# Kernel tuning notes

Hardware: AMD Instinct MI355X
Metric: run time of the kernel (lower is better)

The kernel has to match this reference:

```python
import jax, jax.numpy as jnp
import numpy as np

N_SEQ = 250000
L = 40
C_IN = 20
K = 4
D = 32
N_BAGS = 100
SEQ_PER_BAG = N_SEQ // N_BAGS


def _param(key, shape):
    # matches torch init: normal(0, sqrt(1/prod(shape)))
    return jax.random.normal(key, shape, dtype=jnp.float32) * np.sqrt(1.0 / np.prod(shape))


def setup_inputs() -> dict:
    key = jax.random.key(0)
    ks = jax.random.split(key, 16)
    inp = {
        "x": jax.random.normal(ks[0], (N_SEQ, L, C_IN), dtype=jnp.float32),
        # equal-size bags: 100 bags of 2500 sequences (sum == N_SEQ)
        "n_per_bag": jnp.full((N_BAGS,), SEQ_PER_BAG, dtype=jnp.int32),
        # CNN: two conv1d layers, kernel shape (K, in, out) for 'NWC'/'WIO'
        "conv1_w": _param(ks[1], (K, C_IN, D)), "conv1_b": jnp.zeros((D,), jnp.float32),
        "conv2_w": _param(ks[2], (K, D, D)),    "conv2_b": jnp.zeros((D,), jnp.float32),
        # attention MLP: 32->32->32->1
        "att_w1": _param(ks[3], (D, D)), "att_b1": jnp.zeros((D,), jnp.float32),
        "att_w2": _param(ks[4], (D, D)), "att_b2": jnp.zeros((D,), jnp.float32),
        "att_w3": _param(ks[5], (D, 1)), "att_b3": jnp.zeros((1,), jnp.float32),
        # output net A: 32->32->21, output net B: 32->32->40
        "outA_w1": _param(ks[6], (D, D)),  "outA_b1": jnp.zeros((D,), jnp.float32),
        "outA_w2": _param(ks[7], (D, 21)), "outA_b2": jnp.zeros((21,), jnp.float32),
        "outB_w1": _param(ks[8], (D, D)),  "outB_b1": jnp.zeros((D,), jnp.float32),
        "outB_w2": _param(ks[9], (D, 40)), "outB_b2": jnp.zeros((40,), jnp.float32),
    }
    return inp


def _conv1d_nwc(x, w, b):
    # x: (N, L, Cin), w: (K, Cin, Cout) -> (N, L-K+1, Cout), VALID padding
    return jax.lax.conv_general_dilated(
        x, w, window_strides=(1,), padding="VALID",
        dimension_numbers=("NWC", "WIO", "NWC")) + b


def _forward(x, n_per_bag, conv1_w, conv1_b, conv2_w, conv2_b,
             att_w1, att_b1, att_w2, att_b2, att_w3, att_b3,
             outA_w1, outA_b1, outA_w2, outA_b2,
             outB_w1, outB_b1, outB_w2, outB_b2):
    selu = jax.nn.selu
    # --- sequence embedding CNN (dropout = identity in eval) ---
    h = selu(_conv1d_nwc(x, conv1_w, conv1_b))          # (N, L-3, D)
    h = selu(_conv1d_nwc(h, conv2_w, conv2_b))          # (N, L-6, D)
    seq_embed = h.max(axis=1)                           # (N, D)
    # --- attention scores ---
    a = selu(seq_embed @ att_w1 + att_b1)
    a = selu(a @ att_w2 + att_b2)
    scores = (a @ att_w3 + att_b3)[:, 0]                # (N,)
    # --- per-bag segment softmax + weighted-sum pooling ---
    seg = jnp.repeat(jnp.arange(N_BAGS, dtype=jnp.int32), np.asarray(n_per_bag),
                     total_repeat_length=seq_embed.shape[0])
    seg_max = jax.ops.segment_max(scores, seg, num_segments=N_BAGS)
    e = jnp.exp(scores - seg_max[seg])
    denom = jax.ops.segment_sum(e, seg, num_segments=N_BAGS)
    w = e / denom[seg]                                  # (N,)
    pooled = jax.ops.segment_sum(seq_embed * w[:, None], seg,
                                 num_segments=N_BAGS)   # (N_BAGS, D)
    # --- output networks (n_layers=2: one hidden SELU layer + final, then sigmoid) ---
    pa = jax.nn.sigmoid(selu(pooled @ outA_w1 + outA_b1) @ outA_w2 + outA_b2)
    pb = jax.nn.sigmoid(selu(pooled @ outB_w1 + outB_b1) @ outB_w2 + outB_b2)
    return pa, pb


def reference(x, n_per_bag, conv1_w, conv1_b, conv2_w, conv2_b,
              att_w1, att_b1, att_w2, att_b2, att_w3, att_b3,
              outA_w1, outA_b1, outA_w2, outA_b2,
              outB_w1, outB_b1, outB_w2, outB_b2):
    return _forward(x, n_per_bag, conv1_w, conv1_b, conv2_w, conv2_b,
                    att_w1, att_b1, att_w2, att_b2, att_w3, att_b3,
                    outA_w1, outA_b1, outA_w2, outA_b2,
                    outB_w1, outB_b1, outB_w2, outB_b2)
```

## Files before the change

kernel.cpp:

```cpp
#include <hip/hip_runtime.h>

#define N_SEQ 250000
#define LSEQ  40
#define CIN   20
#define KW    4
#define DCH   32
#define L1    37
#define L2    34
#define N_BAGS 100
#define SPB   2500
#define S_BLK 8
#define R1    (S_BLK * L1)
#define R2    (S_BLK * L2)
#define T1C   10
#define T2C   9
#define H1S   36
#define H2S   33

typedef _Float16 f16;
typedef _Float16 f16x8 __attribute__((ext_vector_type(8)));
typedef _Float16 f16x4 __attribute__((ext_vector_type(4)));
typedef float    f32x16 __attribute__((ext_vector_type(16)));

__device__ __forceinline__ float selu_f(float x) {
  float e = 1.6732632423543772f * (__expf(x) - 1.0f);
  return 1.0507009873554805f * ((x > 0.0f) ? x : e);
}

__global__ __launch_bounds__(256) void prep_kernel(
    const float* __restrict__ w1, const float* __restrict__ w2,
    const float* __restrict__ aw1, const float* __restrict__ aw2,
    f16* __restrict__ w1T, f16* __restrict__ w2T,
    float* __restrict__ aw1T, float* __restrict__ aw2T)
{
  const int tid = threadIdx.x;
  for (int i = tid; i < 32 * 80; i += 256) {
    const int n = i / 80, k = i - n * 80;
    w1T[i] = (f16)w1[k * 32 + n];
  }
  for (int i = tid; i < 32 * 128; i += 256) {
    const int n = i >> 7, k = i & 127;
    w2T[i] = (f16)w2[k * 32 + n];
  }
  for (int i = tid; i < 1024; i += 256) {
    const int d = i >> 5, c = i & 31;
    aw1T[i] = aw1[c * 32 + d];
    aw2T[i] = aw2[c * 32 + d];
  }
}

__global__ __launch_bounds__(256, 4) void seq_kernel(
    const float* __restrict__ x,
    const f16*  __restrict__ w1T, const float* __restrict__ b1,
    const f16*  __restrict__ w2T, const float* __restrict__ b2,
    const float* __restrict__ aw1T, const float* __restrict__ ab1,
    const float* __restrict__ aw2T, const float* __restrict__ ab2,
    const float* __restrict__ aw3, const float* __restrict__ ab3,
    f16* __restrict__ se_out, float* __restrict__ sc_out)
{
  __shared__ __align__(16) f16 reg1[R2 * H2S];
  __shared__ __align__(16) f16 reg2[R1 * H1S];

  f16* xs = reg1;
  f16* h2 = reg1;
  f16* h1 = reg2;
  float* sebuf = (float*)reg2;
  float* abuf  = sebuf + 256;

  const int tid  = threadIdx.x;
  const int lane = tid & 63;
  const int wave = tid >> 6;
  const int m    = lane & 31;
  const int half = lane >> 5;
  const int seq0 = blockIdx.x * S_BLK;

  f16x8 bf1[5], bf2[8];
  {
    const f16x8* w1t8 = (const f16x8*)w1T;
    const f16x8* w2t8 = (const f16x8*)w2T;
    #pragma unroll
    for (int kc = 0; kc < 5; kc++) bf1[kc] = w1t8[m * 10 + kc * 2 + half];
    #pragma unroll
    for (int kc = 0; kc < 8; kc++) bf2[kc] = w2t8[m * 16 + kc * 2 + half];
  }
  const float b1v = b1[m], b2v = b2[m];

  {
    const float4* xg = (const float4*)(x + (size_t)blockIdx.x * (S_BLK * LSEQ * CIN));
    for (int i = tid; i < S_BLK * LSEQ * CIN / 4; i += 256) {
      const float4 v = xg[i];
      f16x4 h; h[0] = (f16)v.x; h[1] = (f16)v.y; h[2] = (f16)v.z; h[3] = (f16)v.w;
      *(f16x4*)&xs[i * 4] = h;
    }
  }
  __syncthreads();

  for (int tile = wave; tile < T1C; tile += 4) {
    const unsigned r  = tile * 32 + m;
    const unsigned rc = (r < R1) ? r : (R1 - 1);
    const unsigned s  = rc / L1, l = rc - s * L1;
    const f16* arow = &xs[(s * LSEQ + l) * CIN];
    f32x16 acc;
    #pragma unroll
    for (int i = 0; i < 16; i++) acc[i] = b1v;
    #pragma unroll
    for (int kc = 0; kc < 5; kc++) {
      const int e = kc * 16 + half * 8;
      const f16x4 p0 = *(const f16x4*)(arow + e);
      const f16x4 p1 = *(const f16x4*)(arow + e + 4);
      const f16x8 a = __builtin_shufflevector(p0, p1, 0, 1, 2, 3, 4, 5, 6, 7);
      acc = __builtin_amdgcn_mfma_f32_32x32x16_f16(a, bf1[kc], acc, 0, 0, 0);
    }
    #pragma unroll
    for (int reg = 0; reg < 16; reg++) {
      const int rr = tile * 32 + (reg & 3) + 8 * (reg >> 2) + 4 * half;
      if (rr < R1) h1[rr * H1S + m] = (f16)selu_f(acc[reg]);
    }
  }
  __syncthreads();

  for (int tile = wave; tile < T2C; tile += 4) {
    const unsigned r  = tile * 32 + m;
    const unsigned rc = (r < R2) ? r : (R2 - 1);
    const unsigned s  = rc / L2, l = rc - s * L2;
    const f16* abase = &h1[(s * L1 + l) * H1S];
    f32x16 acc;
    #pragma unroll
    for (int i = 0; i < 16; i++) acc[i] = b2v;
    #pragma unroll
    for (int kc = 0; kc < 8; kc++) {
      const int e = (kc >> 1) * H1S + (kc & 1) * 16 + half * 8;
      const f16x4 p0 = *(const f16x4*)(abase + e);
      const f16x4 p1 = *(const f16x4*)(abase + e + 4);
      const f16x8 a = __builtin_shufflevector(p0, p1, 0, 1, 2, 3, 4, 5, 6, 7);
      acc = __builtin_amdgcn_mfma_f32_32x32x16_f16(a, bf2[kc], acc, 0, 0, 0);
    }
    #pragma unroll
    for (int reg = 0; reg < 16; reg++) {
      const int rr = tile * 32 + (reg & 3) + 8 * (reg >> 2) + 4 * half;
      if (rr < R2) h2[rr * H2S + m] = (f16)acc[reg];
    }
  }
  __syncthreads();

  {
    const int s = tid >> 5, d = tid & 31;
    float mx = -3.4e38f;
    for (int l = 0; l < L2; l++) mx = fmaxf(mx, (float)h2[(s * L2 + l) * H2S + d]);
    const float sv = selu_f(mx);
    sebuf[tid] = sv;
    se_out[(size_t)seq0 * DCH + tid] = (f16)sv;
  }
  __syncthreads();

  {
    const int s = tid >> 5, d = tid & 31;
    const float4* wt = (const float4*)aw1T;
    float a = ab1[d];
    #pragma unroll
    for (int c4 = 0; c4 < 8; c4++) {
      const float4 w = wt[d * 8 + c4];
      const float* sb = &sebuf[s * DCH + c4 * 4];
      a = fmaf(sb[0], w.x, a); a = fmaf(sb[1], w.y, a);
      a = fmaf(sb[2], w.z, a); a = fmaf(sb[3], w.w, a);
    }
    abuf[tid] = selu_f(a);
  }
  __syncthreads();

  {
    const int s = tid >> 5, d = tid & 31;
    const float4* wt = (const float4*)aw2T;
    float a = ab2[d];
    #pragma unroll
    for (int c4 = 0; c4 < 8; c4++) {
      const float4 w = wt[d * 8 + c4];
      const float* sb = &abuf[s * DCH + c4 * 4];
      a = fmaf(sb[0], w.x, a); a = fmaf(sb[1], w.y, a);
      a = fmaf(sb[2], w.z, a); a = fmaf(sb[3], w.w, a);
    }
    a = selu_f(a);
    float p = a * aw3[d];
    #pragma unroll
    for (int off = 16; off > 0; off >>= 1) p += __shfl_xor(p, off, 32);
    if (d == 0) sc_out[seq0 + s] = p + ab3[0];
  }
}

__global__ __launch_bounds__(256) void bag_kernel(
    const f16* __restrict__ se, const float* __restrict__ sc,
    const float* __restrict__ aw1, const float* __restrict__ ab1,
    const float* __restrict__ aw2, const float* __restrict__ ab2,
    const float* __restrict__ bw1, const float* __restrict__ bb1,
    const float* __restrict__ bw2, const float* __restrict__ bb2,
    float* __restrict__ out)
{
  const int bag = blockIdx.x, tid = threadIdx.x;
  const size_t base = (size_t)bag * SPB;

  __shared__ float pr[4][33];
  __shared__ float red[33];
  __shared__ float pool[DCH], hA[DCH], hB[DCH];

  float m = -3.4e38f;
  for (int i = tid; i < SPB; i += 256) m = fmaxf(m, sc[base + i]);
  #pragma unroll
  for (int off = 32; off > 0; off >>= 1) m = fmaxf(m, __shfl_xor(m, off, 64));
  if ((tid & 63) == 0) pr[tid >> 6][0] = m;
  __syncthreads();
  const float bagmax = fmaxf(fmaxf(pr[0][0], pr[1][0]), fmaxf(pr[2][0], pr[3][0]));
  __syncthreads();

  float acc[33];
  #pragma unroll
  for (int d = 0; d < 33; d++) acc[d] = 0.0f;
  for (int i = tid; i < SPB; i += 256) {
    const float e = __expf(sc[base + i] - bagmax);
    acc[32] += e;
    const f16* sr = &se[(base + i) * DCH];
    #pragma unroll
    for (int q = 0; q < 8; q++) {
      const f16x4 v = *(const f16x4*)(sr + q * 4);
      #pragma unroll
      for (int j = 0; j < 4; j++) acc[q * 4 + j] = fmaf(e, (float)v[j], acc[q * 4 + j]);
    }
  }
  #pragma unroll
  for (int d = 0; d < 33; d++) {
    float v = acc[d];
    #pragma unroll
    for (int off = 32; off > 0; off >>= 1) v += __shfl_xor(v, off, 64);
    if ((tid & 63) == 0) pr[tid >> 6][d] = v;
  }
  __syncthreads();
  if (tid < 33) red[tid] = pr[0][tid] + pr[1][tid] + pr[2][tid] + pr[3][tid];
  __syncthreads();
  if (tid < DCH) pool[tid] = red[tid] / red[32];
  __syncthreads();

  if (tid < DCH) {
    float a = ab1[tid], b = bb1[tid];
    #pragma unroll
    for (int c = 0; c < DCH; c++) {
      a = fmaf(pool[c], aw1[c * DCH + tid], a);
      b = fmaf(pool[c], bw1[c * DCH + tid], b);
    }
    hA[tid] = selu_f(a);
    hB[tid] = selu_f(b);
  }
  __syncthreads();

  if (tid < 21) {
    float v = ab2[tid];
    #pragma unroll
    for (int d = 0; d < DCH; d++) v = fmaf(hA[d], aw2[d * 21 + tid], v);
    out[bag * 21 + tid] = 1.0f / (1.0f + __expf(-v));
  } else if (tid >= 32 && tid < 72) {
    const int j = tid - 32;
    float v = bb2[j];
    #pragma unroll
    for (int d = 0; d < DCH; d++) v = fmaf(hB[d], bw2[d * 40 + j], v);
    out[N_BAGS * 21 + bag * 40 + j] = 1.0f / (1.0f + __expf(-v));
  }
}

extern "C" void kernel_launch(void* const* d_in, const int* in_sizes, int n_in,
                              void* d_out, int out_size, void* d_ws, size_t ws_size,
                              hipStream_t stream)
{
  const float* x    = (const float*)d_in[0];
  const float* c1w  = (const float*)d_in[2];
  const float* c1b  = (const float*)d_in[3];
  const float* c2w  = (const float*)d_in[4];
  const float* c2b  = (const float*)d_in[5];
  const float* aw1  = (const float*)d_in[6];
  const float* ab1  = (const float*)d_in[7];
  const float* aw2  = (const float*)d_in[8];
  const float* ab2  = (const float*)d_in[9];
  const float* aw3  = (const float*)d_in[10];
  const float* ab3  = (const float*)d_in[11];
  const float* oaw1 = (const float*)d_in[12];
  const float* oab1 = (const float*)d_in[13];
  const float* oaw2 = (const float*)d_in[14];
  const float* oab2 = (const float*)d_in[15];
  const float* obw1 = (const float*)d_in[16];
  const float* obb1 = (const float*)d_in[17];
  const float* obw2 = (const float*)d_in[18];
  const float* obb2 = (const float*)d_in[19];
  float* out = (float*)d_out;

  char* ws = (char*)d_ws;
  f16*   seh  = (f16*)ws;
  float* sc   = (float*)(ws + (size_t)16000000);
  f16*   w1T  = (f16*)(ws + (size_t)17000000);
  f16*   w2T  = w1T + 2560 + 2560;
  float* aw1T = (float*)(ws + (size_t)17000000 + 32768);
  float* aw2T = aw1T + 1024;

  prep_kernel<<<1, 256, 0, stream>>>(c1w, c2w, aw1, aw2, w1T, w2T, aw1T, aw2T);
  seq_kernel<<<N_SEQ / S_BLK, 256, 0, stream>>>(x, w1T, c1b, w2T, c2b,
                                                aw1T, ab1, aw2T, ab2, aw3, ab3,
                                                seh, sc);
  bag_kernel<<<N_BAGS, 256, 0, stream>>>(seh, sc, oaw1, oab1, oaw2, oab2,
                                         obw1, obb1, obw2, obb2, out);
}
```

Measured before the change: 1.442 ms.

## Fuse max-pooling into conv2 MFMA epilogue and widen seq blocks to 512 threads

The conv2 output is no longer written to shared memory. Each tile now reduces its accumulator rows straight into per-sequence partial maxima, stored in a small shared table, and the final max combines at most two tiles per sequence. The attention MLP takes its inputs through wave shuffles instead of shared buffers, which removes two barriers. The block grows to 512 threads (8 waves) so every conv tile gets its own wave, at the cost of idle waves in the tail stages and higher register pressure under launch_bounds(512,8).

```diff
diff --git a/kernel.cpp b/kernel.cpp
--- a/kernel.cpp
+++ b/kernel.cpp
@@ -10,12 +10,12 @@
 #define N_BAGS 100
 #define SPB   2500
 #define S_BLK 8
+#define NTHR  512
 #define R1    (S_BLK * L1)
 #define R2    (S_BLK * L2)
 #define T1C   10
 #define T2C   9
 #define H1S   36
-#define H2S   33
 
 typedef _Float16 f16;
 typedef _Float16 f16x8 __attribute__((ext_vector_type(8)));
@@ -49,7 +49,7 @@
   }
 }
 
-__global__ __launch_bounds__(256, 4) void seq_kernel(
+__global__ __launch_bounds__(NTHR, 8) void seq_kernel(
     const float* __restrict__ x,
     const f16*  __restrict__ w1T, const float* __restrict__ b1,
     const f16*  __restrict__ w2T, const float* __restrict__ b2,
@@ -58,14 +58,9 @@
     const float* __restrict__ aw3, const float* __restrict__ ab3,
     f16* __restrict__ se_out, float* __restrict__ sc_out)
 {
-  __shared__ __align__(16) f16 reg1[R2 * H2S];
-  __shared__ __align__(16) f16 reg2[R1 * H1S];
-
-  f16* xs = reg1;
-  f16* h2 = reg1;
-  f16* h1 = reg2;
-  float* sebuf = (float*)reg2;
-  float* abuf  = sebuf + 256;
+  __shared__ __align__(16) f16 xs[S_BLK * LSEQ * CIN];
+  __shared__ __align__(16) f16 h1[R1 * H1S];
+  __shared__ float pt[T2C][2][DCH];
 
   const int tid  = threadIdx.x;
   const int lane = tid & 63;
@@ -87,7 +82,7 @@
 
   {
     const float4* xg = (const float4*)(x + (size_t)blockIdx.x * (S_BLK * LSEQ * CIN));
-    for (int i = tid; i < S_BLK * LSEQ * CIN / 4; i += 256) {
+    for (int i = tid; i < S_BLK * LSEQ * CIN / 4; i += NTHR) {
       const float4 v = xg[i];
       f16x4 h; h[0] = (f16)v.x; h[1] = (f16)v.y; h[2] = (f16)v.z; h[3] = (f16)v.w;
       *(f16x4*)&xs[i * 4] = h;
@@ -95,7 +90,7 @@
   }
   __syncthreads();
 
-  for (int tile = wave; tile < T1C; tile += 4) {
+  for (int tile = wave; tile < T1C; tile += 8) {
     const unsigned r  = tile * 32 + m;
     const unsigned rc = (r < R1) ? r : (R1 - 1);
     const unsigned s  = rc / L1, l = rc - s * L1;
@@ -119,7 +114,7 @@
   }
   __syncthreads();
 
-  for (int tile = wave; tile < T2C; tile += 4) {
+  for (int tile = wave; tile < T2C; tile += 8) {
     const unsigned r  = tile * 32 + m;
     const unsigned rc = (r < R2) ? r : (R2 - 1);
     const unsigned s  = rc / L2, l = rc - s * L2;
@@ -135,52 +130,56 @@
       const f16x8 a = __builtin_shufflevector(p0, p1, 0, 1, 2, 3, 4, 5, 6, 7);
       acc = __builtin_amdgcn_mfma_f32_32x32x16_f16(a, bf2[kc], acc, 0, 0, 0);
     }
+    const int s0  = (tile * 32 * 241) >> 13;
+    const int bnd = (s0 + 1) * L2;
+    float mx0 = -3.4e38f, mx1 = -3.4e38f;
     #pragma unroll
     for (int reg = 0; reg < 16; reg++) {
-      const int rr = tile * 32 + (reg & 3) + 8 * (reg >> 2) + 4 * half;
-      if (rr < R2) h2[rr * H2S + m] = (f16)acc[reg];
-    }
-  }
-  __syncthreads();
-
-  {
+      int rr = tile * 32 + (reg & 3) + 8 * (reg >> 2) + 4 * half;
+      if (rr > R2 - 1) rr = R2 - 1;
+      if (rr < bnd) mx0 = fmaxf(mx0, acc[reg]);
+      else          mx1 = fmaxf(mx1, acc[reg]);
+    }
+    mx0 = fmaxf(mx0, __shfl_xor(mx0, 32, 64));
+    mx1 = fmaxf(mx1, __shfl_xor(mx1, 32, 64));
+    if (half == 0) { pt[tile][0][m] = mx0; pt[tile][1][m] = mx1; }
+  }
+  __syncthreads();
+
+  if (tid < S_BLK * DCH) {
     const int s = tid >> 5, d = tid & 31;
-    float mx = -3.4e38f;
-    for (int l = 0; l < L2; l++) mx = fmaxf(mx, (float)h2[(s * L2 + l) * H2S + d]);
+    const int tA = (s * L2) >> 5;
+    const int tB = (s * L2 + L2 - 1) >> 5;
+    const int sA = ((tA << 5) * 241) >> 13;
+    const int sB = ((tB << 5) * 241) >> 13;
+    const float mx = fmaxf(pt[tA][(s == sA) ? 0 : 1][d],
+                           pt[tB][(s == sB) ? 0 : 1][d]);
     const float sv = selu_f(mx);
-    sebuf[tid] = sv;
     se_out[(size_t)seq0 * DCH + tid] = (f16)sv;
-  }
-  __syncthreads();
-
-  {
-    const int s = tid >> 5, d = tid & 31;
-    const float4* wt = (const float4*)aw1T;
+
+    const float4* wt1 = (const float4*)aw1T;
     float a = ab1[d];
     #pragma unroll
     for (int c4 = 0; c4 < 8; c4++) {
-      const float4 w = wt[d * 8 + c4];
-      const float* sb = &sebuf[s * DCH + c4 * 4];
-      a = fmaf(sb[0], w.x, a); a = fmaf(sb[1], w.y, a);
-      a = fmaf(sb[2], w.z, a); a = fmaf(sb[3], w.w, a);
-    }
-    abuf[tid] = selu_f(a);
-  }
-  __syncthreads();
-
-  {
-    const int s = tid >> 5, d = tid & 31;
-    const float4* wt = (const float4*)aw2T;
-    float a = ab2[d];
+      const float4 w = wt1[d * 8 + c4];
+      a = fmaf(__shfl(sv, c4 * 4 + 0, 32), w.x, a);
+      a = fmaf(__shfl(sv, c4 * 4 + 1, 32), w.y, a);
+      a = fmaf(__shfl(sv, c4 * 4 + 2, 32), w.z, a);
+      a = fmaf(__shfl(sv, c4 * 4 + 3, 32), w.w, a);
+    }
+    const float av = selu_f(a);
+
+    const float4* wt2 = (const float4*)aw2T;
+    float a2 = ab2[d];
     #pragma unroll
     for (int c4 = 0; c4 < 8; c4++) {
-      const float4 w = wt[d * 8 + c4];
-      const float* sb = &abuf[s * DCH + c4 * 4];
-      a = fmaf(sb[0], w.x, a); a = fmaf(sb[1], w.y, a);
-      a = fmaf(sb[2], w.z, a); a = fmaf(sb[3], w.w, a);
-    }
-    a = selu_f(a);
-    float p = a * aw3[d];
+      const float4 w = wt2[d * 8 + c4];
+      a2 = fmaf(__shfl(av, c4 * 4 + 0, 32), w.x, a2);
+      a2 = fmaf(__shfl(av, c4 * 4 + 1, 32), w.y, a2);
+      a2 = fmaf(__shfl(av, c4 * 4 + 2, 32), w.z, a2);
+      a2 = fmaf(__shfl(av, c4 * 4 + 3, 32), w.w, a2);
+    }
+    float p = selu_f(a2) * aw3[d];
     #pragma unroll
     for (int off = 16; off > 0; off >>= 1) p += __shfl_xor(p, off, 32);
     if (d == 0) sc_out[seq0 + s] = p + ab3[0];
@@ -298,9 +297,9 @@
   float* aw2T = aw1T + 1024;
 
   prep_kernel<<<1, 256, 0, stream>>>(c1w, c2w, aw1, aw2, w1T, w2T, aw1T, aw2T);
-  seq_kernel<<<N_SEQ / S_BLK, 256, 0, stream>>>(x, w1T, c1b, w2T, c2b,
-                                                aw1T, ab1, aw2T, ab2, aw3, ab3,
-                                                seh, sc);
+  seq_kernel<<<N_SEQ / S_BLK, NTHR, 0, stream>>>(x, w1T, c1b, w2T, c2b,
+                                                 aw1T, ab1, aw2T, ab2, aw3, ab3,
+                                                 seh, sc);
   bag_kernel<<<N_BAGS, 256, 0, stream>>>(seh, sc, oaw1, oab1, oaw2, oab2,
                                          obw1, obb1, obw2, obb2, out);
 }
```

New measurement: 2.124 ms. 1.47x slower.
